# Kernel tuning notes

Measured on AMD Instinct MI355X. Metric: run time of the kernel, lower is better.

The kernel has to match this reference:

```python
import jax, jax.numpy as jnp
import numpy as np

B, OBS, H, M, L1, T, A = 16384, 376, 512, 8, 3, 50, 17  # L1 = num_layers - 1
LOG_SQRT_2PI = 0.5 * np.log(2.0 * np.pi).astype(np.float32)


def setup_inputs() -> dict:
    key = jax.random.key(0)
    ks = jax.random.split(key, 16)
    s = lambda fan: 1.0 / np.sqrt(fan).astype(np.float32)
    return {
        "x": jax.random.normal(ks[0], (B, OBS), jnp.float32),
        "task_idx": jax.random.randint(ks[1], (B,), 0, T, jnp.int64),
        "enc_W1": jax.random.normal(ks[2], (OBS, H), jnp.float32) * s(OBS),
        "enc_b1": jnp.zeros((H,), jnp.float32),
        "enc_W2": jax.random.normal(ks[3], (H, H), jnp.float32) * s(H),
        "enc_b2": jnp.zeros((H,), jnp.float32),
        "task_emb": jax.random.normal(ks[4], (T, H), jnp.float32),
        "a_rW": jax.random.normal(ks[5], (L1, H, M * M), jnp.float32) * s(H),
        "a_rb": jnp.zeros((L1, M * M), jnp.float32),
        "c_rW": jax.random.normal(ks[6], (L1, H, M * M), jnp.float32) * s(H),
        "c_rb": jnp.zeros((L1, M * M), jnp.float32),
        "a_W": jax.random.normal(ks[7], (L1, M, H, H), jnp.float32) * s(H),
        "a_b": jnp.zeros((L1, M, H), jnp.float32),
        "a_Wf": jax.random.normal(ks[8], (M, H, A), jnp.float32) * 0.01,
        "a_bf": jnp.zeros((M, A), jnp.float32),
        "c_W": jax.random.normal(ks[9], (L1, M, H, H), jnp.float32) * s(H),
        "c_b": jnp.zeros((L1, M, H), jnp.float32),
        "c_Wf": jax.random.normal(ks[10], (M, H, 1), jnp.float32) * s(H),
        "c_bf": jnp.zeros((M, 1), jnp.float32),
        "actor_logstd": jnp.zeros((1, A), jnp.float32),
    }


def _routing(context, rW, rb):
    # context: [B,H]; rW: [L1,H,M*M] -> list of [B,M,M] softmax routing probs
    rel = jax.nn.relu(context)
    probs = []
    for l in range(L1):
        logits = (rel @ rW[l] + rb[l]).reshape(-1, M, M)
        probs.append(jax.nn.softmax(logits, axis=2))
    return probs


def _base(f_s, probs, W, b, Wf, bf):
    # f_s: [B,H]; W: [L1,M,H,H]; Wf: [M,H,out]
    g = jnp.broadcast_to(f_s[:, None, :], (f_s.shape[0], M, H))  # [B,M,H]
    for l in range(L1):
        outs = jax.nn.relu(jnp.einsum("bmh,mhk->bmk", g, W[l]) + b[l])  # [B,M,H]
        g = jnp.einsum("bij,bjh->bih", probs[l], outs)  # soft combine
    final = jnp.einsum("bmh,mhk->bmk", g, Wf) + bf  # [B,M,out]
    return final.sum(axis=1)


def reference(x, task_idx, enc_W1, enc_b1, enc_W2, enc_b2, task_emb,
              a_rW, a_rb, c_rW, c_rb, a_W, a_b, a_Wf, a_bf,
              c_W, c_b, c_Wf, c_bf, actor_logstd):
    f_s = jnp.tanh(jnp.tanh(x @ enc_W1 + enc_b1) @ enc_W2 + enc_b2)  # [B,H]
    h_z = task_emb[task_idx]  # [B,H]
    context = f_s * h_z

    value = _base(f_s, _routing(context, c_rW, c_rb), c_W, c_b, c_Wf, c_bf)  # [B,1]
    mean = _base(f_s, _routing(context, a_rW, a_rb), a_W, a_b, a_Wf, a_bf)   # [B,A]

    # deterministic action (sample=False): action = mean
    logstd = jnp.broadcast_to(actor_logstd, mean.shape)
    log_prob = (-logstd - LOG_SQRT_2PI).sum(axis=1)          # N.log_prob(mean).sum(1)
    entropy = (0.5 + LOG_SQRT_2PI + logstd).sum(axis=1)
    # concat (action, log_prob, entropy, value) -> [B, A+3]
    return jnp.concatenate([mean, log_prob[:, None], entropy[:, None], value], axis=1)
```

## Files before the change

### kernel.cpp

```cpp
#include <hip/hip_runtime.h>
#include <hip/hip_bf16.h>

typedef float f32x4 __attribute__((ext_vector_type(4)));
typedef float f32x2 __attribute__((ext_vector_type(2)));
typedef int   i32x4 __attribute__((ext_vector_type(4)));
typedef int   i32x8 __attribute__((ext_vector_type(8)));

#define LOG_SQRT_2PI 0.91893853320467274f

static constexpr int BSZ  = 16384;
static constexpr int OBSN = 376;
static constexpr int HD   = 512;
static constexpr int NACT = 17;

__device__ __forceinline__ unsigned char f2fp8(float v) {
  return (unsigned char)(__builtin_amdgcn_cvt_pk_fp8_f32(v, v, 0, false) & 0xFF);
}

__device__ __forceinline__ void gl16(const unsigned char* g, unsigned char* l) {
  __builtin_amdgcn_global_load_lds((const __attribute__((address_space(1))) void*)g,
                                   (__attribute__((address_space(3))) void*)l, 16, 0, 0);
}

__device__ __forceinline__ void xcd_map(int id, int gx, int gy, int& bx, int& by, int& bz) {
  int p = id & 7, l = id >> 3;
  bx = l % gx;
  int g = (l / gx) * 8 + p;
  by = g % gy;
  bz = g / gy;
}


__global__ void k_cvt_pad8(const float* __restrict__ src, unsigned char* __restrict__ dst) {
  long i = (long)blockIdx.x * 256 + threadIdx.x;
  if (i >= (long)BSZ * HD) return;
  long r = i >> 9;
  int  c = (int)(i & 511);
  dst[i] = f2fp8(c < OBSN ? src[r * OBSN + c] : 0.f);
}

__global__ void k_packT8(const float* __restrict__ src, unsigned char* __restrict__ dst,
                         int K, int N, int Kpad, long sstride, long dstride, float scale) {
  __shared__ float t[32][33];
  src += (long)blockIdx.z * sstride;
  dst += (long)blockIdx.z * dstride;
  int k0 = blockIdx.y * 32, n0 = blockIdx.x * 32;
#pragma unroll
  for (int ii = 0; ii < 4; ++ii) {
    int i = ii * 8 + threadIdx.y;
    int k = k0 + i, n = n0 + threadIdx.x;
    t[i][threadIdx.x] = (k < K && n < N) ? src[(long)k * N + n] : 0.f;
  }
  __syncthreads();
#pragma unroll
  for (int ii = 0; ii < 4; ++ii) {
    int i = ii * 8 + threadIdx.y;
    int n = n0 + i, k = k0 + threadIdx.x;
    if (n < N && k < Kpad) dst[(long)n * Kpad + k] = f2fp8(scale * t[threadIdx.x][i]);
  }
}

__global__ void k_packwF(const float* __restrict__ aW, const float* __restrict__ cW,
                         unsigned char* __restrict__ dst) {
  long i = (long)blockIdx.x * 256 + threadIdx.x;
  if (i >= (long)48 * 262144) return;
  int z = (int)(i >> 18);
  int rem = (int)(i & 262143);
  int k = rem >> 9, n = rem & 511;
  int layer = z >> 4, zz = z & 15, net = zz >> 3, m = zz & 7;
  const float* src = (net ? aW : cW) + (long)(layer * 8 + m) * 262144;
  float v = src[(long)k * 512 + n];
  int t = k >> 7, nb = n >> 4;
  int lane = ((k >> 5) & 3) * 16 + (n & 15);
  long off = ((((long)z * 4 + t) * 32 + nb) * 64 + lane) * 32 + (k & 31);
  dst[off] = f2fp8(16.f * v);
}

__global__ void k_pack_lb(const float* __restrict__ a_b, const float* __restrict__ c_b,
                          float* __restrict__ lb) {
  int i = blockIdx.x * 256 + threadIdx.x;
  if (i >= 24576) return;
  int layer = i >> 13, zz = (i >> 9) & 15, n = i & 511;
  int net = zz >> 3, m = zz & 7;
  lb[i] = (net ? a_b : c_b)[(layer * 8 + m) * 512 + n];
}

__global__ void k_packwf8(const float* __restrict__ aWf, const float* __restrict__ cWf,
                          unsigned char* __restrict__ dsta, unsigned char* __restrict__ dstc) {
  int i = blockIdx.x * 256 + threadIdx.x;
  int n = i >> 12, kn = i & 4095;
  int hb = kn >> 9, rem = kn & 511, m = rem >> 6, u = kn & 63;
  int ko = m * 512 + hb * 64 + u;
  dsta[i] = (n < NACT) ? f2fp8(64.f * aWf[(long)ko * NACT + n]) : (unsigned char)0;
  dstc[i] = (n < 1)    ? f2fp8(64.f * cWf[ko])                  : (unsigned char)0;
}

__global__ void k_pack_rb(const float* __restrict__ a_rb, const float* __restrict__ c_rb,
                          float* __restrict__ rb) {
  int i = threadIdx.x;
  rb[i] = (i < 192) ? a_rb[i] : c_rb[i - 192];
}

__global__ void k_sum_bf(const float* __restrict__ a_bf, const float* __restrict__ c_bf,
                         float* __restrict__ sa, float* __restrict__ sc) {
  int a = threadIdx.x;
  if (a < NACT) { float s = 0.f; for (int m = 0; m < 8; ++m) s += a_bf[m * NACT + a]; sa[a] = s; }
  if (a == 0)   { float s = 0.f; for (int m = 0; m < 8; ++m) s += c_bf[m];            sc[0] = s; }
}

__global__ void k_initout(const float* __restrict__ bfa, const float* __restrict__ bfc,
                          float* __restrict__ out) {
  long i = (long)blockIdx.x * 256 + threadIdx.x;
  if (i >= (long)BSZ * 20) return;
  int o = (int)(i % 20);
  out[i] = (o < NACT) ? bfa[o] : (o == 19 ? bfc[0] : 0.f);
}

template <int OP>
__global__ __launch_bounds__(256, 4)
void k_gemm8(const unsigned char* __restrict__ A, const unsigned char* __restrict__ Bt,
             void* __restrict__ Cv, const float* __restrict__ bias,
             int N, int K, int lda, int ldc, int gx, int gy,
             const int* __restrict__ tidx, const float* __restrict__ temb,
             unsigned char* __restrict__ out2) {
  __shared__ alignas(16) unsigned char sA[128 * 128];
  __shared__ alignas(16) unsigned char sB[128 * 128];
  int bx, by, z;
  xcd_map(blockIdx.x, gx, gy, bx, by, z);
  const int tid  = threadIdx.x;
  const int wave = tid >> 6, lane = tid & 63;
  const int wr = (wave >> 1) * 64, wc = (wave & 1) * 64;
  const int row0 = by * 128, col0 = bx * 128;
  const int lcol = lane & 15, quad = lane >> 4;
  const int sw7 = lcol & 7;
  const int c0 = ((2 * quad)     ^ sw7) * 16;
  const int c1 = ((2 * quad + 1) ^ sw7) * 16;
  const int raA0 = (wr + lcol) * 128 + c0, raA1 = (wr + lcol) * 128 + c1;
  const int rbB0 = (wc + lcol) * 128 + c0, rbB1 = (wc + lcol) * 128 + c1;
  int aOff[4], bOff[4];
#pragma unroll
  for (int i = 0; i < 4; ++i) {
    int u = i * 256 + tid;
    int r = u >> 3, gc = (u & 7) ^ (r & 7);
    aOff[i] = (row0 + r) * lda + gc * 16;
    bOff[i] = (col0 + r) * K + gc * 16;
  }

  f32x4 acc[4][4] = {};

  for (int kt = 0; kt < K; kt += 128) {
#pragma unroll
    for (int i = 0; i < 4; ++i) gl16(A + aOff[i] + kt, &sA[i * 4096 + tid * 16]);
#pragma unroll
    for (int i = 0; i < 4; ++i) gl16(Bt + bOff[i] + kt, &sB[i * 4096 + tid * 16]);
    __syncthreads();
    i32x8 bv[4];
#pragma unroll
    for (int ni = 0; ni < 4; ++ni) {
      i32x4 blo = *(const i32x4*)&sB[rbB0 + ni * 2048];
      i32x4 bhi = *(const i32x4*)&sB[rbB1 + ni * 2048];
      bv[ni] = (i32x8){blo[0], blo[1], blo[2], blo[3], bhi[0], bhi[1], bhi[2], bhi[3]};
    }
#pragma unroll
    for (int mi = 0; mi < 4; ++mi) {
      i32x4 alo = *(const i32x4*)&sA[raA0 + mi * 2048];
      i32x4 ahi = *(const i32x4*)&sA[raA1 + mi * 2048];
      i32x8 af = (i32x8){alo[0], alo[1], alo[2], alo[3], ahi[0], ahi[1], ahi[2], ahi[3]};
#pragma unroll
      for (int ni = 0; ni < 4; ++ni)
        acc[mi][ni] = __builtin_amdgcn_mfma_scale_f32_16x16x128_f8f6f4(
            bv[ni], af, acc[mi][ni], 0, 0, 0, 0x7F, 0, 0x7F);
    }
    __syncthreads();
  }

#pragma unroll
  for (int ni = 0; ni < 4; ++ni) {
    int colb = col0 + wc + ni * 16 + quad * 4;
    if (colb >= N) continue;
    float4 bw = *(const float4*)&bias[colb];
#pragma unroll
    for (int mi = 0; mi < 4; ++mi) {
      int rowg = row0 + wr + mi * 16 + lcol;
      float v0 = acc[mi][ni][0] * 0.0625f + bw.x;
      float v1 = acc[mi][ni][1] * 0.0625f + bw.y;
      float v2 = acc[mi][ni][2] * 0.0625f + bw.z;
      float v3 = acc[mi][ni][3] * 0.0625f + bw.w;
      long idx = (long)rowg * ldc + colb;
      if (OP == 1) {
        float t0 = tanhf(v0), t1 = tanhf(v1), t2 = tanhf(v2), t3 = tanhf(v3);
        unsigned d = __builtin_amdgcn_cvt_pk_fp8_f32(t0, t1, 0, false);
        d = __builtin_amdgcn_cvt_pk_fp8_f32(t2, t3, d, true);
        *(unsigned*)&((unsigned char*)Cv)[idx] = d;
      } else if (OP == 5) {
        float t0 = tanhf(v0), t1 = tanhf(v1), t2 = tanhf(v2), t3 = tanhf(v3);
        unsigned d = __builtin_amdgcn_cvt_pk_fp8_f32(t0, t1, 0, false);
        d = __builtin_amdgcn_cvt_pk_fp8_f32(t2, t3, d, true);
        *(unsigned*)&((unsigned char*)Cv)[idx] = d;
        int tk = tidx[rowg];
        float4 te = *(const float4*)&temb[(long)tk * HD + colb];
        unsigned e = __builtin_amdgcn_cvt_pk_fp8_f32(fmaxf(t0 * te.x, 0.f), fmaxf(t1 * te.y, 0.f), 0, false);
        e = __builtin_amdgcn_cvt_pk_fp8_f32(fmaxf(t2 * te.z, 0.f), fmaxf(t3 * te.w, 0.f), e, true);
        *(unsigned*)&out2[idx] = e;
      } else if (OP == 4) {
        float mx = fmaxf(fmaxf(v0, v1), fmaxf(v2, v3));
        mx = fmaxf(mx, __shfl_xor(mx, 16));
        float e0 = __expf(v0 - mx), e1 = __expf(v1 - mx), e2 = __expf(v2 - mx), e3 = __expf(v3 - mx);
        float s = e0 + e1 + e2 + e3;
        s += __shfl_xor(s, 16);
        float inv = 1.f / s;
        *(float4*)&((float*)Cv)[idx] = make_float4(e0 * inv, e1 * inv, e2 * inv, e3 * inv);
      }
    }
  }
}

template <int AMODE, int HEAD>
__global__ __launch_bounds__(512, 4)
void k_gemmF(const unsigned char* __restrict__ A, const unsigned char* __restrict__ Wp,
             const float* __restrict__ lb, const float* __restrict__ probs,
             unsigned char* __restrict__ g, int gy, int poffC, int poffA,
             const unsigned char* __restrict__ Wfc, const unsigned char* __restrict__ Wfa,
             float* __restrict__ outp) {
  __shared__ alignas(16) unsigned char sL[AMODE ? 65536 : 32768];
  int hb, slab, net;
  xcd_map(blockIdx.x, 8, gy, hb, slab, net);
  const int tid = threadIdx.x;
  const int w = tid >> 6, lane = tid & 63;
  const int lcol = lane & 15, quad = lane >> 4;
  const int ln3 = lane >> 3, sl = lane & 7;
  const int row0 = slab * 64;
  const int h0 = hb * 64;
  const int sw7 = lcol & 7;
  const int c0 = ((2 * quad)     ^ sw7) * 16;
  const int c1 = ((2 * quad + 1) ^ sw7) * 16;
  const int ch = sl ^ ln3;
  const unsigned char* wbase =
      Wp + (((long)(net * 8 + w) * 4 * 32 + hb * 4) * 64 + lane) * 32;

  f32x4 acc[4][4] = {};

  if (AMODE == 0) {
#pragma unroll
    for (int i = 0; i < 4; ++i) {
      int vb = w * 4 + i;
      int rr = (vb & 7) * 8 + ln3;
      gl16(A + (row0 + rr) * 512 + (vb >> 3) * 128 + ch * 16, &sL[(vb * 64 + lane) * 16]);
    }
    __syncthreads();
#pragma unroll
    for (int t = 0; t < 4; ++t) {
      i32x8 bv[4];
#pragma unroll
      for (int ni = 0; ni < 4; ++ni) {
        i32x4 lo = *(const i32x4*)(wbase + t * 65536 + ni * 2048);
        i32x4 hi = *(const i32x4*)(wbase + t * 65536 + ni * 2048 + 16);
        bv[ni] = (i32x8){lo[0], lo[1], lo[2], lo[3], hi[0], hi[1], hi[2], hi[3]};
      }
#pragma unroll
      for (int mi = 0; mi < 4; ++mi) {
        int ra = t * 8192 + (mi * 16 + lcol) * 128;
        i32x4 lo = *(const i32x4*)&sL[ra + c0];
        i32x4 hi = *(const i32x4*)&sL[ra + c1];
        i32x8 af = (i32x8){lo[0], lo[1], lo[2], lo[3], hi[0], hi[1], hi[2], hi[3]};
#pragma unroll
        for (int ni = 0; ni < 4; ++ni)
          acc[mi][ni] = __builtin_amdgcn_mfma_scale_f32_16x16x128_f8f6f4(
              bv[ni], af, acc[mi][ni], 0, 0, 0, 0x7F, 0, 0x7F);
      }
    }
  } else {
    const unsigned char* abase = A + (long)(row0 + ln3) * 8192 + net * 4096 +
                                 w * 64 + (ch >> 2) * 512 + (ch & 3) * 16;
    unsigned char* dbase = &sL[w * 8192 + lane * 16];
#pragma unroll 1
    for (int t = 0; t < 4; ++t) {
#pragma unroll
      for (int i = 0; i < 8; ++i)
        gl16(abase + i * 8 * 8192 + t * 1024, dbase + i * 1024);
      i32x8 bv[4];
#pragma unroll
      for (int ni = 0; ni < 4; ++ni) {
        i32x4 lo = *(const i32x4*)(wbase + t * 65536 + ni * 2048);
        i32x4 hi = *(const i32x4*)(wbase + t * 65536 + ni * 2048 + 16);
        bv[ni] = (i32x8){lo[0], lo[1], lo[2], lo[3], hi[0], hi[1], hi[2], hi[3]};
      }
      asm volatile("s_waitcnt vmcnt(0)" ::: "memory");
      __builtin_amdgcn_sched_barrier(0);
#pragma unroll
      for (int mi = 0; mi < 4; ++mi) {
        int ra = w * 8192 + (mi * 16 + lcol) * 128;
        i32x4 lo = *(const i32x4*)&sL[ra + c0];
        i32x4 hi = *(const i32x4*)&sL[ra + c1];
        i32x8 af = (i32x8){lo[0], lo[1], lo[2], lo[3], hi[0], hi[1], hi[2], hi[3]};
#pragma unroll
        for (int ni = 0; ni < 4; ++ni)
          acc[mi][ni] = __builtin_amdgcn_mfma_scale_f32_16x16x128_f8f6f4(
              bv[ni], af, acc[mi][ni], 0, 0, 0, 0x7F, 0, 0x7F);
      }
    }
  }

  __syncthreads();

#pragma unroll
  for (int ni = 0; ni < 4; ++ni) {
    int col = ni * 16 + quad * 4;
    float4 bw = *(const float4*)&lb[(net * 8 + w) * 512 + h0 + col];
    int sd = ni * 4 + quad;
#pragma unroll
    for (int mi = 0; mi < 4; ++mi) {
      int row = mi * 16 + lcol;
      float v0 = fmaxf(acc[mi][ni][0] * 0.0625f + bw.x, 0.f);
      float v1 = fmaxf(acc[mi][ni][1] * 0.0625f + bw.y, 0.f);
      float v2 = fmaxf(acc[mi][ni][2] * 0.0625f + bw.z, 0.f);
      float v3 = fmaxf(acc[mi][ni][3] * 0.0625f + bw.w, 0.f);
      unsigned d = __builtin_amdgcn_cvt_pk_fp8_f32(v0, v1, 0, false);
      d = __builtin_amdgcn_cvt_pk_fp8_f32(v2, v3, d, true);
      *(unsigned*)&sL[w * 4096 + row * 64 + ((sd ^ (row & 14)) << 2)] = d;
    }
  }
  __syncthreads();

  const int poff = net ? poffA : poffC;
#pragma unroll
  for (int k = 0; k < 8; ++k) {
    const int r = k * 8 + ln3;
    const float* pr = &probs[(long)(row0 + r) * 384 + poff + w * 8];
    float4 pA = *(const float4*)pr;
    float4 pB = *(const float4*)(pr + 4);
    float p8[8] = {pA.x, pA.y, pA.z, pA.w, pB.x, pB.y, pB.z, pB.w};
    float ga[8] = {};
#pragma unroll
    for (int j = 0; j < 8; ++j) {
      uint2 o2 = *(const uint2*)&sL[j * 4096 + r * 64 + (((sl * 2) ^ (r & 14)) << 2)];
      float pw = p8[j];
      f32x2 a0 = __builtin_amdgcn_cvt_pk_f32_fp8(o2.x, false);
      f32x2 a1 = __builtin_amdgcn_cvt_pk_f32_fp8(o2.x, true);
      f32x2 a2 = __builtin_amdgcn_cvt_pk_f32_fp8(o2.y, false);
      f32x2 a3 = __builtin_amdgcn_cvt_pk_f32_fp8(o2.y, true);
      ga[0] += pw * a0.x; ga[1] += pw * a0.y; ga[2] += pw * a1.x; ga[3] += pw * a1.y;
      ga[4] += pw * a2.x; ga[5] += pw * a2.y; ga[6] += pw * a3.x; ga[7] += pw * a3.y;
    }
    unsigned lo = __builtin_amdgcn_cvt_pk_fp8_f32(ga[0], ga[1], 0, false);
    lo = __builtin_amdgcn_cvt_pk_fp8_f32(ga[2], ga[3], lo, true);
    unsigned hi = __builtin_amdgcn_cvt_pk_fp8_f32(ga[4], ga[5], 0, false);
    hi = __builtin_amdgcn_cvt_pk_fp8_f32(ga[6], ga[7], hi, true);
    if (HEAD) {
      *(uint2*)&sL[32768 + w * 4096 + r * 64 + (((sl * 2) ^ (r & 14)) << 2)] =
          make_uint2(lo, hi);
    } else {
      *(uint2*)&g[(long)(row0 + r) * 8192 + net * 4096 + hb * 512 + w * 64 + sl * 8] =
          make_uint2(lo, hi);
    }
  }

  if (HEAD) {
    __syncthreads();
    const unsigned char* Wf = net ? Wfa : Wfc;
    const int ooff = net ? 0 : 19;
    const int mi = w & 3, kh = w >> 2;
    const int hrow = mi * 16 + lcol;
    f32x4 hacc[2] = {};
#pragma unroll
    for (int ks = 0; ks < 8; ++ks) {
      int j = kh * 4 + (ks >> 1);
      int u = (ks & 1) * 32 + quad * 8;
      int sd = u >> 2;
      long af = *(const long*)&sL[32768 + j * 4096 + hrow * 64 + ((sd ^ (hrow & 14)) << 2)];
      int kglob = hb * 512 + kh * 256 + ks * 32 + quad * 8;
      long bv0 = *(const long*)&Wf[(long)lcol * 4096 + kglob];
      hacc[0] = __builtin_amdgcn_mfma_f32_16x16x32_fp8_fp8(af, bv0, hacc[0], 0, 0, 0);
      if (net) {
        long bv1 = *(const long*)&Wf[(long)(16 + lcol) * 4096 + kglob];
        hacc[1] = __builtin_amdgcn_mfma_f32_16x16x32_fp8_fp8(af, bv1, hacc[1], 0, 0, 0);
      }
    }
    const int NOUTn = net ? NACT : 1;
#pragma unroll
    for (int ni = 0; ni < 2; ++ni) {
      if (ni == 1 && !net) break;
      int col = ni * 16 + lcol;
      if (col >= NOUTn) continue;
#pragma unroll
      for (int rr = 0; rr < 4; ++rr) {
        int row = row0 + mi * 16 + quad * 4 + rr;
        atomicAdd(&outp[(long)row * 20 + ooff + col], hacc[ni][rr] * 0.015625f);
      }
    }
  }
}

__global__ void k_logstd(const float* __restrict__ ls, float* __restrict__ out) {
  float lp = 0.f, ent = 0.f;
#pragma unroll
  for (int a = 0; a < NACT; ++a) {
    float v = ls[a];
    lp  += -v - LOG_SQRT_2PI;
    ent += 0.5f + LOG_SQRT_2PI + v;
  }
  long b = (long)blockIdx.x * 256 + threadIdx.x;
  if (b < BSZ) { out[b * 20 + 17] = lp; out[b * 20 + 18] = ent; }
}


extern "C" void kernel_launch(void* const* d_in, const int* in_sizes, int n_in,
                              void* d_out, int out_size, void* d_ws, size_t ws_size,
                              hipStream_t stream) {
  const float* x        = (const float*)d_in[0];
  const int*   task_idx = (const int*)d_in[1];
  const float* enc_W1   = (const float*)d_in[2];
  const float* enc_b1   = (const float*)d_in[3];
  const float* enc_W2   = (const float*)d_in[4];
  const float* enc_b2   = (const float*)d_in[5];
  const float* task_emb = (const float*)d_in[6];
  const float* a_rW     = (const float*)d_in[7];
  const float* a_rb     = (const float*)d_in[8];
  const float* c_rW     = (const float*)d_in[9];
  const float* c_rb     = (const float*)d_in[10];
  const float* a_W      = (const float*)d_in[11];
  const float* a_b      = (const float*)d_in[12];
  const float* a_Wf     = (const float*)d_in[13];
  const float* a_bf     = (const float*)d_in[14];
  const float* c_W      = (const float*)d_in[15];
  const float* c_b      = (const float*)d_in[16];
  const float* c_Wf     = (const float*)d_in[17];
  const float* c_bf     = (const float*)d_in[18];
  const float* logstd   = (const float*)d_in[19];
  float* out = (float*)d_out;

  char* ws = (char*)d_ws;
  size_t off = 0;
  auto carve = [&](size_t bytes) {
    char* p = ws + off;
    off += (bytes + 255) & ~(size_t)255;
    return p;
  };
  unsigned char* W8 = (unsigned char*)carve((size_t)48 * 262144);
  unsigned char* W1T8 = (unsigned char*)carve((size_t)512 * 512);
  unsigned char* W2T8 = (unsigned char*)carve((size_t)512 * 512);
  unsigned char* rWT8 = (unsigned char*)carve((size_t)384 * 512);
  float* rball = (float*)carve(384 * 4);
  float* lb    = (float*)carve(3 * 16 * 512 * 4);
  unsigned char* WfaT8 = (unsigned char*)carve((size_t)32 * 4096);
  unsigned char* WfcT8 = (unsigned char*)carve((size_t)32 * 4096);
  float* bfa   = (float*)carve(128 * 4);
  float* bfc   = (float*)carve(128 * 4);
  unsigned char* fs8 = (unsigned char*)carve((size_t)BSZ * HD);
  float* lgt   = (float*)carve((size_t)BSZ * 384 * 4);

  size_t remain = (ws_size > off) ? (ws_size - off) : 0;
  int Bc = 2048;
  for (int cand = BSZ; cand > 2048; cand >>= 1)
    if ((size_t)2 * cand * 8192 <= remain) { Bc = cand; break; }
  size_t half = (size_t)Bc * 8192;
  unsigned char* bufA8 = (unsigned char*)carve(half);
  unsigned char* bufB8 = (unsigned char*)carve(half);
  unsigned char* x8   = bufA8;
  unsigned char* h18  = bufB8;
  unsigned char* rel8 = bufA8;

  dim3 tb(32, 8);

  k_cvt_pad8<<<(int)(((long)BSZ * HD + 255) / 256), 256, 0, stream>>>(x, x8);
  k_packT8<<<dim3(16, 16, 1), tb, 0, stream>>>(enc_W1, W1T8, OBSN, 512, 512, 0, 0, 16.f);
  k_packT8<<<dim3(16, 16, 1), tb, 0, stream>>>(enc_W2, W2T8, 512, 512, 512, 0, 0, 16.f);
  k_packT8<<<dim3(2, 16, 3),  tb, 0, stream>>>(a_rW, rWT8,             512, 64, 512, 512 * 64, 64 * 512, 16.f);
  k_packT8<<<dim3(2, 16, 3),  tb, 0, stream>>>(c_rW, rWT8 + 192 * 512, 512, 64, 512, 512 * 64, 64 * 512, 16.f);
  k_packwF<<<(int)(((long)48 * 262144 + 255) / 256), 256, 0, stream>>>(a_W, c_W, W8);
  k_pack_lb<<<96, 256, 0, stream>>>(a_b, c_b, lb);
  k_packwf8<<<512, 256, 0, stream>>>(a_Wf, c_Wf, WfaT8, WfcT8);
  k_pack_rb<<<1, 384, 0, stream>>>(a_rb, c_rb, rball);
  k_sum_bf<<<1, 32, 0, stream>>>(a_bf, c_bf, bfa, bfc);
  k_initout<<<(int)(((long)BSZ * 20 + 255) / 256), 256, 0, stream>>>(bfa, bfc, out);

  const int GY = BSZ / 128;
  k_gemm8<1><<<4 * GY, 256, 0, stream>>>(x8, W1T8, h18, enc_b1, 512, 512, 512, 512,
                                         4, GY, nullptr, nullptr, nullptr);
  k_gemm8<5><<<4 * GY, 256, 0, stream>>>(h18, W2T8, fs8, enc_b2, 512, 512, 512, 512,
                                         4, GY, task_idx, task_emb, rel8);
  k_gemm8<4><<<3 * GY, 256, 0, stream>>>(rel8, rWT8, lgt, rball, 384, 512, 512, 384,
                                         3, GY, nullptr, nullptr, nullptr);

  const size_t wlz = (size_t)16 * 262144;
  for (int c0 = 0; c0 < BSZ; c0 += Bc) {
    const unsigned char* fs_c = fs8 + (long)c0 * 512;
    const float* pr_c  = lgt + (long)c0 * 384;
    float*       out_c = out + (long)c0 * 20;
    const int gyF = Bc / 64;

    k_gemmF<0, 0><<<16 * gyF, 512, 0, stream>>>(fs_c, W8, lb, pr_c, bufA8, gyF, 192, 0,
                                                nullptr, nullptr, nullptr);
    k_gemmF<1, 0><<<16 * gyF, 512, 0, stream>>>(bufA8, W8 + wlz, lb + 8192, pr_c, bufB8,
                                                gyF, 192 + 64, 64, nullptr, nullptr, nullptr);
    k_gemmF<1, 1><<<16 * gyF, 512, 0, stream>>>(bufB8, W8 + 2 * wlz, lb + 16384, pr_c, bufA8,
                                                gyF, 192 + 128, 128, WfcT8, WfaT8, out_c);
  }

  k_logstd<<<BSZ / 256, 256, 0, stream>>>(logstd, out);
}
```

Before: 739.5 us.

## Fuse encoder GEMMs and routing GEMM into one kernel keeping activations in LDS

The two encoder layers, the context/relu step and the routing-logit GEMM with softmax are merged into one kernel per 64-row tile. Intermediate activations stay in shared memory and the weights are read straight from global memory in a pre-swizzled fragment layout, so the h1 and rel8 round trips to global memory go away. The small packing, bias-sum, init and logstd kernels are also folded into fewer launches. The trade-off is that every block re-reads the full weight matrices from L2, and large launch bounds may limit occupancy.

Measured after the change: 807.9 us. 1.09x slower.

```diff
diff --git a/kernel.cpp b/kernel.cpp
--- a/kernel.cpp
+++ b/kernel.cpp
@@ -39,25 +39,20 @@
   dst[i] = f2fp8(c < OBSN ? src[r * OBSN + c] : 0.f);
 }
 
-__global__ void k_packT8(const float* __restrict__ src, unsigned char* __restrict__ dst,
-                         int K, int N, int Kpad, long sstride, long dstride, float scale) {
-  __shared__ float t[32][33];
-  src += (long)blockIdx.z * sstride;
-  dst += (long)blockIdx.z * dstride;
-  int k0 = blockIdx.y * 32, n0 = blockIdx.x * 32;
-#pragma unroll
-  for (int ii = 0; ii < 4; ++ii) {
-    int i = ii * 8 + threadIdx.y;
-    int k = k0 + i, n = n0 + threadIdx.x;
-    t[i][threadIdx.x] = (k < K && n < N) ? src[(long)k * N + n] : 0.f;
-  }
-  __syncthreads();
-#pragma unroll
-  for (int ii = 0; ii < 4; ++ii) {
-    int i = ii * 8 + threadIdx.y;
-    int n = n0 + i, k = k0 + threadIdx.x;
-    if (n < N && k < Kpad) dst[(long)n * Kpad + k] = f2fp8(scale * t[threadIdx.x][i]);
-  }
+__global__ void k_packTF(const float* __restrict__ src, unsigned char* __restrict__ dst,
+                         int K, int N, int NB, long sstride, long total) {
+  long i = (long)blockIdx.x * 256 + threadIdx.x;
+  if (i >= total) return;
+  int kk = (int)(i & 31);
+  long j = i >> 5;
+  int lane = (int)(j & 63); j >>= 6;
+  int nb = (int)(j % NB); j /= NB;
+  int t = (int)(j & 3); j >>= 2;
+  int z = (int)j;
+  int n = nb * 16 + (lane & 15);
+  int k = t * 128 + ((lane >> 4) & 3) * 32 + kk;
+  float v = (k < K && n < N) ? src[(long)z * sstride + (long)k * N + n] : 0.f;
+  dst[i] = f2fp8(16.f * v);
 }
 
 __global__ void k_packwF(const float* __restrict__ aW, const float* __restrict__ cW,
@@ -76,140 +71,172 @@
   dst[off] = f2fp8(16.f * v);
 }
 
-__global__ void k_pack_lb(const float* __restrict__ a_b, const float* __restrict__ c_b,
-                          float* __restrict__ lb) {
+__global__ void k_packmisc(const float* __restrict__ a_b, const float* __restrict__ c_b,
+                           const float* __restrict__ aWf, const float* __restrict__ cWf,
+                           const float* __restrict__ a_rb, const float* __restrict__ c_rb,
+                           float* __restrict__ lb, unsigned char* __restrict__ dsta,
+                           unsigned char* __restrict__ dstc, float* __restrict__ rb) {
   int i = blockIdx.x * 256 + threadIdx.x;
-  if (i >= 24576) return;
-  int layer = i >> 13, zz = (i >> 9) & 15, n = i & 511;
-  int net = zz >> 3, m = zz & 7;
-  lb[i] = (net ? a_b : c_b)[(layer * 8 + m) * 512 + n];
-}
-
-__global__ void k_packwf8(const float* __restrict__ aWf, const float* __restrict__ cWf,
-                          unsigned char* __restrict__ dsta, unsigned char* __restrict__ dstc) {
-  int i = blockIdx.x * 256 + threadIdx.x;
-  int n = i >> 12, kn = i & 4095;
-  int hb = kn >> 9, rem = kn & 511, m = rem >> 6, u = kn & 63;
-  int ko = m * 512 + hb * 64 + u;
-  dsta[i] = (n < NACT) ? f2fp8(64.f * aWf[(long)ko * NACT + n]) : (unsigned char)0;
-  dstc[i] = (n < 1)    ? f2fp8(64.f * cWf[ko])                  : (unsigned char)0;
-}
-
-__global__ void k_pack_rb(const float* __restrict__ a_rb, const float* __restrict__ c_rb,
-                          float* __restrict__ rb) {
-  int i = threadIdx.x;
-  rb[i] = (i < 192) ? a_rb[i] : c_rb[i - 192];
-}
-
-__global__ void k_sum_bf(const float* __restrict__ a_bf, const float* __restrict__ c_bf,
-                         float* __restrict__ sa, float* __restrict__ sc) {
-  int a = threadIdx.x;
-  if (a < NACT) { float s = 0.f; for (int m = 0; m < 8; ++m) s += a_bf[m * NACT + a]; sa[a] = s; }
-  if (a == 0)   { float s = 0.f; for (int m = 0; m < 8; ++m) s += c_bf[m];            sc[0] = s; }
-}
-
-__global__ void k_initout(const float* __restrict__ bfa, const float* __restrict__ bfc,
-                          float* __restrict__ out) {
+  if (i < 24576) {
+    int layer = i >> 13, zz = (i >> 9) & 15, n = i & 511;
+    int net = zz >> 3, m = zz & 7;
+    lb[i] = (net ? a_b : c_b)[(layer * 8 + m) * 512 + n];
+  } else if (i < 24576 + 131072) {
+    int j = i - 24576;
+    int n = j >> 12, kn = j & 4095;
+    int hb = kn >> 9, rem = kn & 511, m = rem >> 6, u = kn & 63;
+    int ko = m * 512 + hb * 64 + u;
+    dsta[j] = (n < NACT) ? f2fp8(64.f * aWf[(long)ko * NACT + n]) : (unsigned char)0;
+    dstc[j] = (n < 1)    ? f2fp8(64.f * cWf[ko])                  : (unsigned char)0;
+  } else if (i < 24576 + 131072 + 384) {
+    int j = i - 24576 - 131072;
+    rb[j] = (j < 192) ? a_rb[j] : c_rb[j - 192];
+  }
+}
+
+__global__ void k_initout2(const float* __restrict__ a_bf, const float* __restrict__ c_bf,
+                           const float* __restrict__ ls, float* __restrict__ out) {
   long i = (long)blockIdx.x * 256 + threadIdx.x;
   if (i >= (long)BSZ * 20) return;
   int o = (int)(i % 20);
-  out[i] = (o < NACT) ? bfa[o] : (o == 19 ? bfc[0] : 0.f);
-}
-
-template <int OP>
-__global__ __launch_bounds__(256, 4)
-void k_gemm8(const unsigned char* __restrict__ A, const unsigned char* __restrict__ Bt,
-             void* __restrict__ Cv, const float* __restrict__ bias,
-             int N, int K, int lda, int ldc, int gx, int gy,
-             const int* __restrict__ tidx, const float* __restrict__ temb,
-             unsigned char* __restrict__ out2) {
-  __shared__ alignas(16) unsigned char sA[128 * 128];
-  __shared__ alignas(16) unsigned char sB[128 * 128];
-  int bx, by, z;
-  xcd_map(blockIdx.x, gx, gy, bx, by, z);
-  const int tid  = threadIdx.x;
-  const int wave = tid >> 6, lane = tid & 63;
-  const int wr = (wave >> 1) * 64, wc = (wave & 1) * 64;
-  const int row0 = by * 128, col0 = bx * 128;
+  float v = 0.f;
+  if (o < NACT) {
+    for (int m = 0; m < 8; ++m) v += a_bf[m * NACT + o];
+  } else if (o == 19) {
+    for (int m = 0; m < 8; ++m) v += c_bf[m];
+  } else if (o == 17) {
+    for (int a = 0; a < NACT; ++a) v += -ls[a] - LOG_SQRT_2PI;
+  } else {
+    for (int a = 0; a < NACT; ++a) v += 0.5f + LOG_SQRT_2PI + ls[a];
+  }
+  out[i] = v;
+}
+
+__global__ __launch_bounds__(512, 2)
+void k_enc(const unsigned char* __restrict__ x8,
+           const unsigned char* __restrict__ W1F, const unsigned char* __restrict__ W2F,
+           const unsigned char* __restrict__ rWF,
+           const float* __restrict__ b1, const float* __restrict__ b2,
+           const float* __restrict__ rb,
+           const int* __restrict__ tidx, const float* __restrict__ temb,
+           unsigned char* __restrict__ fs8, float* __restrict__ probs) {
+  __shared__ alignas(16) unsigned char sL[32768];
+  const int tid = threadIdx.x;
+  const int w = tid >> 6, lane = tid & 63;
   const int lcol = lane & 15, quad = lane >> 4;
+  const int ln3 = lane >> 3, sl = lane & 7;
+  const int row0 = blockIdx.x * 64;
   const int sw7 = lcol & 7;
   const int c0 = ((2 * quad)     ^ sw7) * 16;
   const int c1 = ((2 * quad + 1) ^ sw7) * 16;
-  const int raA0 = (wr + lcol) * 128 + c0, raA1 = (wr + lcol) * 128 + c1;
-  const int rbB0 = (wc + lcol) * 128 + c0, rbB1 = (wc + lcol) * 128 + c1;
-  int aOff[4], bOff[4];
+  const int ch = sl ^ ln3;
+
 #pragma unroll
   for (int i = 0; i < 4; ++i) {
-    int u = i * 256 + tid;
-    int r = u >> 3, gc = (u & 7) ^ (r & 7);
-    aOff[i] = (row0 + r) * lda + gc * 16;
-    bOff[i] = (col0 + r) * K + gc * 16;
-  }
-
-  f32x4 acc[4][4] = {};
-
-  for (int kt = 0; kt < K; kt += 128) {
-#pragma unroll
-    for (int i = 0; i < 4; ++i) gl16(A + aOff[i] + kt, &sA[i * 4096 + tid * 16]);
-#pragma unroll
-    for (int i = 0; i < 4; ++i) gl16(Bt + bOff[i] + kt, &sB[i * 4096 + tid * 16]);
-    __syncthreads();
-    i32x8 bv[4];
+    int vb = w * 4 + i;
+    int rr = (vb & 7) * 8 + ln3;
+    gl16(x8 + (long)(row0 + rr) * 512 + (vb >> 3) * 128 + ch * 16, &sL[(vb * 64 + lane) * 16]);
+  }
+  __syncthreads();
+
+  f32x4 acc[4][4];
+  auto gemm = [&](const unsigned char* wb0, int tstr) {
+#pragma unroll
+    for (int mi = 0; mi < 4; ++mi)
+#pragma unroll
+      for (int ni = 0; ni < 4; ++ni) acc[mi][ni] = (f32x4){0.f, 0.f, 0.f, 0.f};
+#pragma unroll
+    for (int t = 0; t < 4; ++t) {
+      i32x8 bv[4];
+#pragma unroll
+      for (int ni = 0; ni < 4; ++ni) {
+        const unsigned char* wb = wb0 + (long)t * tstr + ni * 2048 + lane * 32;
+        i32x4 lo = *(const i32x4*)wb;
+        i32x4 hi = *(const i32x4*)(wb + 16);
+        bv[ni] = (i32x8){lo[0], lo[1], lo[2], lo[3], hi[0], hi[1], hi[2], hi[3]};
+      }
+#pragma unroll
+      for (int mi = 0; mi < 4; ++mi) {
+        int ra = t * 8192 + (mi * 16 + lcol) * 128;
+        i32x4 lo = *(const i32x4*)&sL[ra + c0];
+        i32x4 hi = *(const i32x4*)&sL[ra + c1];
+        i32x8 af = (i32x8){lo[0], lo[1], lo[2], lo[3], hi[0], hi[1], hi[2], hi[3]};
+#pragma unroll
+        for (int ni = 0; ni < 4; ++ni)
+          acc[mi][ni] = __builtin_amdgcn_mfma_scale_f32_16x16x128_f8f6f4(
+              bv[ni], af, acc[mi][ni], 0, 0, 0, 0x7F, 0, 0x7F);
+      }
+    }
+  };
+
+  gemm(W1F + w * 8192, 65536);
+  __syncthreads();
+#pragma unroll
+  for (int ni = 0; ni < 4; ++ni) {
+    int colb = w * 64 + ni * 16 + quad * 4;
+    float4 bw = *(const float4*)&b1[colb];
+    int tc = (w * 4 + ni) >> 3, chc = (w * 4 + ni) & 7;
+#pragma unroll
+    for (int mi = 0; mi < 4; ++mi) {
+      int row = mi * 16 + lcol;
+      float t0 = tanhf(acc[mi][ni][0] * 0.0625f + bw.x);
+      float t1 = tanhf(acc[mi][ni][1] * 0.0625f + bw.y);
+      float t2 = tanhf(acc[mi][ni][2] * 0.0625f + bw.z);
+      float t3 = tanhf(acc[mi][ni][3] * 0.0625f + bw.w);
+      unsigned d = __builtin_amdgcn_cvt_pk_fp8_f32(t0, t1, 0, false);
+      d = __builtin_amdgcn_cvt_pk_fp8_f32(t2, t3, d, true);
+      *(unsigned*)&sL[tc * 8192 + row * 128 + ((chc ^ (row & 7)) << 4) + quad * 4] = d;
+    }
+  }
+  __syncthreads();
+
+  gemm(W2F + w * 8192, 65536);
+  __syncthreads();
+#pragma unroll
+  for (int ni = 0; ni < 4; ++ni) {
+    int colb = w * 64 + ni * 16 + quad * 4;
+    float4 bw = *(const float4*)&b2[colb];
+    int tc = (w * 4 + ni) >> 3, chc = (w * 4 + ni) & 7;
+#pragma unroll
+    for (int mi = 0; mi < 4; ++mi) {
+      int row = mi * 16 + lcol;
+      int rowg = row0 + row;
+      float t0 = tanhf(acc[mi][ni][0] * 0.0625f + bw.x);
+      float t1 = tanhf(acc[mi][ni][1] * 0.0625f + bw.y);
+      float t2 = tanhf(acc[mi][ni][2] * 0.0625f + bw.z);
+      float t3 = tanhf(acc[mi][ni][3] * 0.0625f + bw.w);
+      unsigned d = __builtin_amdgcn_cvt_pk_fp8_f32(t0, t1, 0, false);
+      d = __builtin_amdgcn_cvt_pk_fp8_f32(t2, t3, d, true);
+      *(unsigned*)&fs8[(long)rowg * 512 + colb] = d;
+      int tk = tidx[rowg];
+      float4 te = *(const float4*)&temb[(long)tk * HD + colb];
+      unsigned e = __builtin_amdgcn_cvt_pk_fp8_f32(fmaxf(t0 * te.x, 0.f), fmaxf(t1 * te.y, 0.f), 0, false);
+      e = __builtin_amdgcn_cvt_pk_fp8_f32(fmaxf(t2 * te.z, 0.f), fmaxf(t3 * te.w, 0.f), e, true);
+      *(unsigned*)&sL[tc * 8192 + row * 128 + ((chc ^ (row & 7)) << 4) + quad * 4] = e;
+    }
+  }
+  __syncthreads();
+
+  if (w < 6) {
+    gemm(rWF + w * 32768, 8192);
 #pragma unroll
     for (int ni = 0; ni < 4; ++ni) {
-      i32x4 blo = *(const i32x4*)&sB[rbB0 + ni * 2048];
-      i32x4 bhi = *(const i32x4*)&sB[rbB1 + ni * 2048];
-      bv[ni] = (i32x8){blo[0], blo[1], blo[2], blo[3], bhi[0], bhi[1], bhi[2], bhi[3]};
-    }
-#pragma unroll
-    for (int mi = 0; mi < 4; ++mi) {
-      i32x4 alo = *(const i32x4*)&sA[raA0 + mi * 2048];
-      i32x4 ahi = *(const i32x4*)&sA[raA1 + mi * 2048];
-      i32x8 af = (i32x8){alo[0], alo[1], alo[2], alo[3], ahi[0], ahi[1], ahi[2], ahi[3]};
-#pragma unroll
-      for (int ni = 0; ni < 4; ++ni)
-        acc[mi][ni] = __builtin_amdgcn_mfma_scale_f32_16x16x128_f8f6f4(
-            bv[ni], af, acc[mi][ni], 0, 0, 0, 0x7F, 0, 0x7F);
-    }
-    __syncthreads();
-  }
-
-#pragma unroll
-  for (int ni = 0; ni < 4; ++ni) {
-    int colb = col0 + wc + ni * 16 + quad * 4;
-    if (colb >= N) continue;
-    float4 bw = *(const float4*)&bias[colb];
-#pragma unroll
-    for (int mi = 0; mi < 4; ++mi) {
-      int rowg = row0 + wr + mi * 16 + lcol;
-      float v0 = acc[mi][ni][0] * 0.0625f + bw.x;
-      float v1 = acc[mi][ni][1] * 0.0625f + bw.y;
-      float v2 = acc[mi][ni][2] * 0.0625f + bw.z;
-      float v3 = acc[mi][ni][3] * 0.0625f + bw.w;
-      long idx = (long)rowg * ldc + colb;
-      if (OP == 1) {
-        float t0 = tanhf(v0), t1 = tanhf(v1), t2 = tanhf(v2), t3 = tanhf(v3);
-        unsigned d = __builtin_amdgcn_cvt_pk_fp8_f32(t0, t1, 0, false);
-        d = __builtin_amdgcn_cvt_pk_fp8_f32(t2, t3, d, true);
-        *(unsigned*)&((unsigned char*)Cv)[idx] = d;
-      } else if (OP == 5) {
-        float t0 = tanhf(v0), t1 = tanhf(v1), t2 = tanhf(v2), t3 = tanhf(v3);
-        unsigned d = __builtin_amdgcn_cvt_pk_fp8_f32(t0, t1, 0, false);
-        d = __builtin_amdgcn_cvt_pk_fp8_f32(t2, t3, d, true);
-        *(unsigned*)&((unsigned char*)Cv)[idx] = d;
-        int tk = tidx[rowg];
-        float4 te = *(const float4*)&temb[(long)tk * HD + colb];
-        unsigned e = __builtin_amdgcn_cvt_pk_fp8_f32(fmaxf(t0 * te.x, 0.f), fmaxf(t1 * te.y, 0.f), 0, false);
-        e = __builtin_amdgcn_cvt_pk_fp8_f32(fmaxf(t2 * te.z, 0.f), fmaxf(t3 * te.w, 0.f), e, true);
-        *(unsigned*)&out2[idx] = e;
-      } else if (OP == 4) {
+      int colb = w * 64 + ni * 16 + quad * 4;
+      float4 bw = *(const float4*)&rb[colb];
+#pragma unroll
+      for (int mi = 0; mi < 4; ++mi) {
+        int rowg = row0 + mi * 16 + lcol;
+        float v0 = acc[mi][ni][0] * 0.0625f + bw.x;
+        float v1 = acc[mi][ni][1] * 0.0625f + bw.y;
+        float v2 = acc[mi][ni][2] * 0.0625f + bw.z;
+        float v3 = acc[mi][ni][3] * 0.0625f + bw.w;
         float mx = fmaxf(fmaxf(v0, v1), fmaxf(v2, v3));
         mx = fmaxf(mx, __shfl_xor(mx, 16));
         float e0 = __expf(v0 - mx), e1 = __expf(v1 - mx), e2 = __expf(v2 - mx), e3 = __expf(v3 - mx);
         float s = e0 + e1 + e2 + e3;
         s += __shfl_xor(s, 16);
         float inv = 1.f / s;
-        *(float4*)&((float*)Cv)[idx] = make_float4(e0 * inv, e1 * inv, e2 * inv, e3 * inv);
+        *(float4*)&probs[(long)rowg * 384 + colb] = make_float4(e0 * inv, e1 * inv, e2 * inv, e3 * inv);
       }
     }
   }
@@ -389,18 +416,6 @@
       }
     }
   }
-}
-
-__global__ void k_logstd(const float* __restrict__ ls, float* __restrict__ out) {
-  float lp = 0.f, ent = 0.f;
-#pragma unroll
-  for (int a = 0; a < NACT; ++a) {
-    float v = ls[a];
-    lp  += -v - LOG_SQRT_2PI;
-    ent += 0.5f + LOG_SQRT_2PI + v;
-  }
-  long b = (long)blockIdx.x * 256 + threadIdx.x;
-  if (b < BSZ) { out[b * 20 + 17] = lp; out[b * 20 + 18] = ent; }
 }
 
 
@@ -436,16 +451,14 @@
     off += (bytes + 255) & ~(size_t)255;
     return p;
   };
-  unsigned char* W8 = (unsigned char*)carve((size_t)48 * 262144);
-  unsigned char* W1T8 = (unsigned char*)carve((size_t)512 * 512);
-  unsigned char* W2T8 = (unsigned char*)carve((size_t)512 * 512);
-  unsigned char* rWT8 = (unsigned char*)carve((size_t)384 * 512);
+  unsigned char* W8  = (unsigned char*)carve((size_t)48 * 262144);
+  unsigned char* W1F = (unsigned char*)carve((size_t)262144);
+  unsigned char* W2F = (unsigned char*)carve((size_t)262144);
+  unsigned char* rWF = (unsigned char*)carve((size_t)2 * 98304);
   float* rball = (float*)carve(384 * 4);
   float* lb    = (float*)carve(3 * 16 * 512 * 4);
   unsigned char* WfaT8 = (unsigned char*)carve((size_t)32 * 4096);
   unsigned char* WfcT8 = (unsigned char*)carve((size_t)32 * 4096);
-  float* bfa   = (float*)carve(128 * 4);
-  float* bfc   = (float*)carve(128 * 4);
   unsigned char* fs8 = (unsigned char*)carve((size_t)BSZ * HD);
   float* lgt   = (float*)carve((size_t)BSZ * 384 * 4);
 
@@ -456,31 +469,20 @@
   size_t half = (size_t)Bc * 8192;
   unsigned char* bufA8 = (unsigned char*)carve(half);
   unsigned char* bufB8 = (unsigned char*)carve(half);
-  unsigned char* x8   = bufA8;
-  unsigned char* h18  = bufB8;
-  unsigned char* rel8 = bufA8;
-
-  dim3 tb(32, 8);
+  unsigned char* x8 = bufA8;
 
   k_cvt_pad8<<<(int)(((long)BSZ * HD + 255) / 256), 256, 0, stream>>>(x, x8);
-  k_packT8<<<dim3(16, 16, 1), tb, 0, stream>>>(enc_W1, W1T8, OBSN, 512, 512, 0, 0, 16.f);
-  k_packT8<<<dim3(16, 16, 1), tb, 0, stream>>>(enc_W2, W2T8, 512, 512, 512, 0, 0, 16.f);
-  k_packT8<<<dim3(2, 16, 3),  tb, 0, stream>>>(a_rW, rWT8,             512, 64, 512, 512 * 64, 64 * 512, 16.f);
-  k_packT8<<<dim3(2, 16, 3),  tb, 0, stream>>>(c_rW, rWT8 + 192 * 512, 512, 64, 512, 512 * 64, 64 * 512, 16.f);
+  k_packTF<<<1024, 256, 0, stream>>>(enc_W1, W1F, OBSN, 512, 32, 0, 262144);
+  k_packTF<<<1024, 256, 0, stream>>>(enc_W2, W2F, 512, 512, 32, 0, 262144);
+  k_packTF<<<384, 256, 0, stream>>>(a_rW, rWF,         512, 64, 4, 512 * 64, 98304);
+  k_packTF<<<384, 256, 0, stream>>>(c_rW, rWF + 98304, 512, 64, 4, 512 * 64, 98304);
   k_packwF<<<(int)(((long)48 * 262144 + 255) / 256), 256, 0, stream>>>(a_W, c_W, W8);
-  k_pack_lb<<<96, 256, 0, stream>>>(a_b, c_b, lb);
-  k_packwf8<<<512, 256, 0, stream>>>(a_Wf, c_Wf, WfaT8, WfcT8);
-  k_pack_rb<<<1, 384, 0, stream>>>(a_rb, c_rb, rball);
-  k_sum_bf<<<1, 32, 0, stream>>>(a_bf, c_bf, bfa, bfc);
-  k_initout<<<(int)(((long)BSZ * 20 + 255) / 256), 256, 0, stream>>>(bfa, bfc, out);
-
-  const int GY = BSZ / 128;
-  k_gemm8<1><<<4 * GY, 256, 0, stream>>>(x8, W1T8, h18, enc_b1, 512, 512, 512, 512,
-                                         4, GY, nullptr, nullptr, nullptr);
-  k_gemm8<5><<<4 * GY, 256, 0, stream>>>(h18, W2T8, fs8, enc_b2, 512, 512, 512, 512,
-                                         4, GY, task_idx, task_emb, rel8);
-  k_gemm8<4><<<3 * GY, 256, 0, stream>>>(rel8, rWT8, lgt, rball, 384, 512, 512, 384,
-                                         3, GY, nullptr, nullptr, nullptr);
+  k_packmisc<<<610, 256, 0, stream>>>(a_b, c_b, a_Wf, c_Wf, a_rb, c_rb,
+                                      lb, WfaT8, WfcT8, rball);
+  k_initout2<<<(int)(((long)BSZ * 20 + 255) / 256), 256, 0, stream>>>(a_bf, c_bf, logstd, out);
+
+  k_enc<<<BSZ / 64, 512, 0, stream>>>(x8, W1F, W2F, rWF, enc_b1, enc_b2, rball,
+                                      task_idx, task_emb, fs8, lgt);
 
   const size_t wlz = (size_t)16 * 262144;
   for (int c0 = 0; c0 < BSZ; c0 += Bc) {
@@ -496,6 +498,4 @@
     k_gemmF<1, 1><<<16 * gyF, 512, 0, stream>>>(bufB8, W8 + 2 * wlz, lb + 16384, pr_c, bufA8,
                                                 gyF, 192 + 128, 128, WfcT8, WfaT8, out_c);
   }
-
-  k_logstd<<<BSZ / 256, 256, 0, stream>>>(logstd, out);
-}
+}
```
